# Performance work log

Hardware: AMD Instinct MI355X
Metric: run time of the kernel (lower is better)

## Reference

```python
import jax, jax.numpy as jnp
import numpy as np

D_MODEL = 1024
NUM_HEADS = 16
D_K = D_MODEL // NUM_HEADS
D_FF = 4096
B, S = 4, 2048
EPS = 1e-5


def _linear_params(key, d_in, d_out):
    # torch nn.Linear default init: U(-1/sqrt(d_in), 1/sqrt(d_in))
    k1, k2 = jax.random.split(key)
    bound = 1.0 / np.sqrt(d_in)
    W = jax.random.uniform(k1, (d_in, d_out), jnp.float32, -bound, bound)
    b = jax.random.uniform(k2, (d_out,), jnp.float32, -bound, bound)
    return W, b


def setup_inputs() -> dict:
    key = jax.random.key(0)
    ks = jax.random.split(key, 8)
    x = jax.random.normal(ks[0], (B, S, D_MODEL), jnp.float32)
    Wq, bq = _linear_params(ks[1], D_MODEL, D_MODEL)
    Wk, bk = _linear_params(ks[2], D_MODEL, D_MODEL)
    Wv, bv = _linear_params(ks[3], D_MODEL, D_MODEL)
    Wo, bo = _linear_params(ks[4], D_MODEL, D_MODEL)
    W1, b1 = _linear_params(ks[5], D_MODEL, D_FF)
    W2, b2 = _linear_params(ks[6], D_FF, D_MODEL)
    ln1_g = jnp.ones((D_MODEL,), jnp.float32)
    ln1_b = jnp.zeros((D_MODEL,), jnp.float32)
    ln2_g = jnp.ones((D_MODEL,), jnp.float32)
    ln2_b = jnp.zeros((D_MODEL,), jnp.float32)
    return dict(x=x, Wq=Wq, bq=bq, Wk=Wk, bk=bk, Wv=Wv, bv=bv, Wo=Wo, bo=bo,
                W1=W1, b1=b1, W2=W2, b2=b2,
                ln1_g=ln1_g, ln1_b=ln1_b, ln2_g=ln2_g, ln2_b=ln2_b)


def _layernorm(x, g, b):
    mu = jnp.mean(x, axis=-1, keepdims=True)
    var = jnp.mean(jnp.square(x - mu), axis=-1, keepdims=True)
    return (x - mu) * jax.lax.rsqrt(var + EPS) * g + b


def _attention(h, Wq, bq, Wk, bk, Wv, bv, Wo, bo):
    b, s, _ = h.shape
    def split_heads(t):  # (b,s,d) -> (b,H,s,dk)
        return t.reshape(b, s, NUM_HEADS, D_K).transpose(0, 2, 1, 3)
    Q = split_heads(h @ Wq + bq)
    K = split_heads(h @ Wk + bk)
    V = split_heads(h @ Wv + bv)
    scores = jnp.einsum('bhqd,bhkd->bhqk', Q, K) / np.sqrt(D_K)
    causal = jnp.tril(jnp.ones((s, s), dtype=bool))  # True = keep
    scores = jnp.where(causal, scores, -jnp.inf)
    attn = jax.nn.softmax(scores, axis=-1)
    out = jnp.einsum('bhqk,bhkd->bhqd', attn, V)
    out = out.transpose(0, 2, 1, 3).reshape(b, s, D_MODEL)
    return out @ Wo + bo


def reference(x, Wq, bq, Wk, bk, Wv, bv, Wo, bo, W1, b1, W2, b2,
              ln1_g, ln1_b, ln2_g, ln2_b):
    # pre-norm residual block
    x = x + _attention(_layernorm(x, ln1_g, ln1_b), Wq, bq, Wk, bk, Wv, bv, Wo, bo)
    h = _layernorm(x, ln2_g, ln2_b)
    x = x + (jax.nn.relu(h @ W1 + b1) @ W2 + b2)
    return x
```

## Files before the change

### kernel.cpp

```cpp
#include <hip/hip_runtime.h>
#include <hip/hip_bf16.h>

typedef __bf16 bf16;
typedef __attribute__((ext_vector_type(8))) __bf16 bf16x8;
typedef __attribute__((ext_vector_type(4))) float f32x4;

#define D_MODEL 1024
#define NHEADS  16
#define DK      64
#define DFF     4096
#define BATCH   4
#define SEQ     2048
#define NTOK    (BATCH*SEQ)

__device__ __forceinline__ void gload16(const bf16* g, bf16* l) {
    __builtin_amdgcn_global_load_lds((const __attribute__((address_space(1))) void*)g,
                                     (__attribute__((address_space(3))) void*)l, 16, 0, 0);
}

__device__ __forceinline__ int pack2(float a, float b) {
    union { bf16 h[2]; int i; } u;
    u.h[0] = (bf16)a; u.h[1] = (bf16)b;
    return u.i;
}

__global__ __launch_bounds__(256) void transpose_cast(
    const float* __restrict__ W, bf16* __restrict__ Wt, int K, int N)
{
    __shared__ float tile[32][33];
    const int tx = threadIdx.x, ty = threadIdx.y;
    const int n0 = blockIdx.x * 32, k0 = blockIdx.y * 32;
#pragma unroll
    for (int i = 0; i < 4; ++i)
        tile[ty + i*8][tx] = W[(size_t)(k0 + ty + i*8) * N + n0 + tx];
    __syncthreads();
#pragma unroll
    for (int i = 0; i < 4; ++i)
        Wt[(size_t)(n0 + ty + i*8) * K + k0 + tx] = (bf16)tile[tx][ty + i*8];
}

__global__ __launch_bounds__(256) void transpose_v(
    const bf16* __restrict__ V, bf16* __restrict__ VT)
{
    __shared__ bf16 t[64][72];
    const int bh = blockIdx.y;
    const int s0 = blockIdx.x * 64;
    const int r  = threadIdx.x >> 2;
    const int c0 = (threadIdx.x & 3) * 16;
    const bf16* Vb = V  + (size_t)bh * SEQ * DK;
    bf16*       Tb = VT + (size_t)bh * DK * SEQ;
#pragma unroll
    for (int i = 0; i < 2; ++i) {
        bf16x8 v = *(const bf16x8*)&Vb[(size_t)(s0 + r) * DK + c0 + i*8];
#pragma unroll
        for (int j = 0; j < 8; ++j) t[c0 + i*8 + j][r] = v[j];
    }
    __syncthreads();
#pragma unroll
    for (int i = 0; i < 2; ++i) {
        bf16x8 o;
#pragma unroll
        for (int j = 0; j < 8; ++j) o[j] = t[r][c0 + i*8 + j];
        *(bf16x8*)&Tb[(size_t)r * SEQ + s0 + c0 + i*8] = o;
    }
}

__global__ __launch_bounds__(256) void ln_kernel(
    const float* __restrict__ x, const float* __restrict__ g,
    const float* __restrict__ beta, bf16* __restrict__ out)
{
    const int row = blockIdx.x, tid = threadIdx.x;
    const f32x4* xr = (const f32x4*)(x + (size_t)row * D_MODEL);
    f32x4 v = xr[tid];
    float s  = v[0] + v[1] + v[2] + v[3];
    float s2 = v[0]*v[0] + v[1]*v[1] + v[2]*v[2] + v[3]*v[3];
#pragma unroll
    for (int off = 32; off > 0; off >>= 1) {
        s  += __shfl_down(s,  off, 64);
        s2 += __shfl_down(s2, off, 64);
    }
    __shared__ float red[8];
    const int wave = tid >> 6, lane = tid & 63;
    if (lane == 0) { red[wave] = s; red[wave + 4] = s2; }
    __syncthreads();
    if (tid == 0) {
        float a = red[0] + red[1] + red[2] + red[3];
        float c = red[4] + red[5] + red[6] + red[7];
        float mu  = a * (1.0f / D_MODEL);
        float var = c * (1.0f / D_MODEL) - mu * mu;
        red[0] = mu;
        red[1] = rsqrtf(var + 1e-5f);
    }
    __syncthreads();
    const float mu = red[0], rs = red[1];
    f32x4 gv = ((const f32x4*)g)[tid];
    f32x4 bv = ((const f32x4*)beta)[tid];
    union { bf16 h[4]; uint2 u; } o;
#pragma unroll
    for (int i = 0; i < 4; ++i) o.h[i] = (bf16)((v[i] - mu) * rs * gv[i] + bv[i]);
    *(uint2*)(out + (size_t)row * D_MODEL + tid * 4) = o.u;
}

template<int EPI>
__global__ __launch_bounds__(256, 2) void gemm_bf16(
    const bf16* __restrict__ A, const bf16* __restrict__ Bt,
    const float* __restrict__ bias, const float* __restrict__ resid,
    void* __restrict__ outp, int M, int N, int K)
{
    __shared__ __align__(16) bf16 As[128 * 32];
    __shared__ __align__(16) bf16 Bs[128 * 32];
    const int tid  = threadIdx.x;
    const int wave = tid >> 6, lane = tid & 63;
    const int quad = lane >> 4, l16 = lane & 15;
    const int wr = wave >> 1, wc = wave & 1;
    const int m0 = blockIdx.y * 128, n0 = blockIdx.x * 128;

    const int r0 = wave * 32 + (lane >> 2);
    const int r1 = r0 + 16;
    const int u0 = ((lane & 3) - ((r0 >> 1) & 3)) & 3;
    const int u1 = ((lane & 3) - ((r1 >> 1) & 3)) & 3;
    const bf16* gA0 = A  + (size_t)(m0 + r0) * K + u0 * 8;
    const bf16* gA1 = A  + (size_t)(m0 + r1) * K + u1 * 8;
    const bf16* gB0 = Bt + (size_t)(n0 + r0) * K + u0 * 8;
    const bf16* gB1 = Bt + (size_t)(n0 + r1) * K + u1 * 8;
    bf16* lA0 = As + wave * 1024;
    bf16* lA1 = As + wave * 1024 + 512;
    bf16* lB0 = Bs + wave * 1024;
    bf16* lB1 = Bs + wave * 1024 + 512;

    int aoff[4], boff[4];
#pragma unroll
    for (int i = 0; i < 4; ++i) {
        const int ra = wr * 64 + i * 16 + l16;
        aoff[i] = ra * 32 + ((quad + ((ra >> 1) & 3)) & 3) * 8;
        const int rb = wc * 64 + i * 16 + l16;
        boff[i] = rb * 32 + ((quad + ((rb >> 1) & 3)) & 3) * 8;
    }

    const f32x4 vzero = {0.f, 0.f, 0.f, 0.f};
    f32x4 acc[4][4];
#pragma unroll
    for (int i = 0; i < 4; ++i)
#pragma unroll
        for (int j = 0; j < 4; ++j) acc[i][j] = vzero;

    for (int k0 = 0; k0 < K; k0 += 32) {
        __syncthreads();
        gload16(gA0 + k0, lA0);
        gload16(gA1 + k0, lA1);
        gload16(gB0 + k0, lB0);
        gload16(gB1 + k0, lB1);
        __syncthreads();
        bf16x8 af[4], bfr[4];
#pragma unroll
        for (int i = 0; i < 4; ++i) af[i]  = *(const bf16x8*)&As[aoff[i]];
#pragma unroll
        for (int j = 0; j < 4; ++j) bfr[j] = *(const bf16x8*)&Bs[boff[j]];
#pragma unroll
        for (int i = 0; i < 4; ++i)
#pragma unroll
            for (int j = 0; j < 4; ++j)
                acc[i][j] = __builtin_amdgcn_mfma_f32_16x16x32_bf16(af[i], bfr[j], acc[i][j], 0, 0, 0);
    }

#pragma unroll
    for (int i = 0; i < 4; ++i) {
#pragma unroll
        for (int j = 0; j < 4; ++j) {
            const int col = n0 + wc * 64 + j * 16 + l16;
            const float bcol = bias[col];
#pragma unroll
            for (int r = 0; r < 4; ++r) {
                const int row = m0 + wr * 64 + i * 16 + quad * 4 + r;
                const float v = acc[i][j][r] + bcol;
                if (EPI == 0) {
                    const int bb = row >> 11, ss = row & (SEQ - 1);
                    const int hh = col >> 6,  dd = col & (DK - 1);
                    ((bf16*)outp)[((size_t)(bb * NHEADS + hh) * SEQ + ss) * DK + dd] = (bf16)v;
                } else if (EPI == 1) {
                    const size_t idx = (size_t)row * N + col;
                    ((float*)outp)[idx] = v + resid[idx];
                } else {
                    ((bf16*)outp)[(size_t)row * N + col] = (bf16)fmaxf(v, 0.f);
                }
            }
        }
    }
}

__global__ __launch_bounds__(256, 2) void attn_kernel(
    const bf16* __restrict__ Q, const bf16* __restrict__ K,
    const bf16* __restrict__ VT, bf16* __restrict__ out)
{
    const int bh = blockIdx.y;
    const int b = bh >> 4, h = bh & 15;
    const int tid  = threadIdx.x;
    const int wave = tid >> 6, lane = tid & 63;
    const int quad = lane >> 4, l16 = lane & 15;

    __shared__ __align__(16) bf16 Ks[128 * 72];
    __shared__ __align__(16) bf16 Vt[64 * 136];

    const bf16* Qb = Q  + (size_t)bh * SEQ * DK;
    const bf16* Kb = K  + (size_t)bh * SEQ * DK;
    const bf16* Vb = VT + (size_t)bh * DK * SEQ;

    const int srcA = (2 * (quad & 1)) * 16 + l16;
    const int srcB = srcA + 16;
    const bool thi = quad >= 2;

    const f32x4 vzero = {0.f, 0.f, 0.f, 0.f};

    for (int half = 0; half < 2; ++half) {
        const int qt = half ? (int)blockIdx.x : 15 - (int)blockIdx.x;
        const int qw = qt * 128 + wave * 32;

        bf16x8 qf[2][2];
#pragma unroll
        for (int qi = 0; qi < 2; ++qi)
#pragma unroll
            for (int kk = 0; kk < 2; ++kk)
                qf[qi][kk] = *(const bf16x8*)&Qb[(size_t)(qw + qi*16 + l16) * DK + kk*32 + quad*8];

        f32x4 Oacc[2][4];
        float m_[2], l_[2];
#pragma unroll
        for (int qi = 0; qi < 2; ++qi) {
            m_[qi] = -3.0e38f; l_[qi] = 0.f;
#pragma unroll
            for (int dj = 0; dj < 4; ++dj) Oacc[qi][dj] = vzero;
        }

        const int ntiles = qt + 1;
        for (int t = 0; t < ntiles; ++t) {
            const int kv0 = t * 128;
            __syncthreads();
            for (int c = tid; c < 1024; c += 256) {
                const int r = c >> 3, u = c & 7;
                *(f32x4*)&Ks[r * 72 + u * 8] = *(const f32x4*)&Kb[(size_t)(kv0 + r) * DK + u * 8];
            }
            for (int c = tid; c < 1024; c += 256) {
                const int r = c >> 4, u = c & 15;
                *(f32x4*)&Vt[r * 136 + u * 8] = *(const f32x4*)&Vb[(size_t)r * SEQ + kv0 + u * 8];
            }
            __syncthreads();

            f32x4 sv[8][2];
#pragma unroll
            for (int kvt = 0; kvt < 8; ++kvt) {
                bf16x8 kf0 = *(const bf16x8*)&Ks[(kvt*16 + l16) * 72 + quad*8];
                bf16x8 kf1 = *(const bf16x8*)&Ks[(kvt*16 + l16) * 72 + 32 + quad*8];
#pragma unroll
                for (int qi = 0; qi < 2; ++qi) {
                    f32x4 tacc = vzero;
                    tacc = __builtin_amdgcn_mfma_f32_16x16x32_bf16(kf0, qf[qi][0], tacc, 0, 0, 0);
                    tacc = __builtin_amdgcn_mfma_f32_16x16x32_bf16(kf1, qf[qi][1], tacc, 0, 0, 0);
                    sv[kvt][qi] = tacc;
                }
            }

            const float scale = 0.125f;
            if (t == qt) {
#pragma unroll
                for (int kvt = 0; kvt < 8; ++kvt)
#pragma unroll
                    for (int qi = 0; qi < 2; ++qi)
#pragma unroll
                        for (int r = 0; r < 4; ++r) {
                            const int kv = kv0 + kvt*16 + quad*4 + r;
                            const int q  = qw + qi*16 + l16;
                            sv[kvt][qi][r] = (kv <= q) ? sv[kvt][qi][r] * scale : -3.0e38f;
                        }
            } else {
#pragma unroll
                for (int kvt = 0; kvt < 8; ++kvt)
#pragma unroll
                    for (int qi = 0; qi < 2; ++qi)
#pragma unroll
                        for (int r = 0; r < 4; ++r) sv[kvt][qi][r] *= scale;
            }

#pragma unroll
            for (int qi = 0; qi < 2; ++qi) {
                float mx = sv[0][qi][0];
#pragma unroll
                for (int kvt = 0; kvt < 8; ++kvt)
#pragma unroll
                    for (int r = 0; r < 4; ++r) mx = fmaxf(mx, sv[kvt][qi][r]);
                mx = fmaxf(mx, __shfl_xor(mx, 16, 64));
                mx = fmaxf(mx, __shfl_xor(mx, 32, 64));
                const float newm  = fmaxf(m_[qi], mx);
                const float alpha = __expf(m_[qi] - newm);
                m_[qi] = newm;
                float rs = 0.f;
#pragma unroll
                for (int kvt = 0; kvt < 8; ++kvt)
#pragma unroll
                    for (int r = 0; r < 4; ++r) {
                        const float p = __expf(sv[kvt][qi][r] - newm);
                        sv[kvt][qi][r] = p;
                        rs += p;
                    }
                rs += __shfl_xor(rs, 16, 64);
                rs += __shfl_xor(rs, 32, 64);
                l_[qi] = l_[qi] * alpha + rs;
#pragma unroll
                for (int dj = 0; dj < 4; ++dj) Oacc[qi][dj] *= alpha;
            }

#pragma unroll
            for (int c2 = 0; c2 < 4; ++c2) {
                bf16x8 vf[4];
#pragma unroll
                for (int dj = 0; dj < 4; ++dj)
                    vf[dj] = *(const bf16x8*)&Vt[(dj*16 + l16) * 136 + c2*32 + quad*8];
#pragma unroll
                for (int qi = 0; qi < 2; ++qi) {
                    const int p00 = pack2(sv[2*c2][qi][0],   sv[2*c2][qi][1]);
                    const int p01 = pack2(sv[2*c2][qi][2],   sv[2*c2][qi][3]);
                    const int p10 = pack2(sv[2*c2+1][qi][0], sv[2*c2+1][qi][1]);
                    const int p11 = pack2(sv[2*c2+1][qi][2], sv[2*c2+1][qi][3]);
                    const int a0 = __shfl(p00, srcA, 64), a1 = __shfl(p01, srcA, 64);
                    const int a2 = __shfl(p10, srcA, 64), a3 = __shfl(p11, srcA, 64);
                    const int b0 = __shfl(p00, srcB, 64), b1 = __shfl(p01, srcB, 64);
                    const int b2 = __shfl(p10, srcB, 64), b3 = __shfl(p11, srcB, 64);
                    union { int i[4]; bf16x8 v; } pf;
                    pf.i[0] = thi ? a2 : a0;
                    pf.i[1] = thi ? a3 : a1;
                    pf.i[2] = thi ? b2 : b0;
                    pf.i[3] = thi ? b3 : b1;
#pragma unroll
                    for (int dj = 0; dj < 4; ++dj)
                        Oacc[qi][dj] = __builtin_amdgcn_mfma_f32_16x16x32_bf16(vf[dj], pf.v, Oacc[qi][dj], 0, 0, 0);
                }
            }
        }

#pragma unroll
        for (int qi = 0; qi < 2; ++qi) {
            const float inv = 1.0f / l_[qi];
            const int q = qw + qi*16 + l16;
#pragma unroll
            for (int dj = 0; dj < 4; ++dj)
#pragma unroll
                for (int r = 0; r < 4; ++r) {
                    const int d = dj*16 + quad*4 + r;
                    out[((size_t)(b * SEQ + q)) * D_MODEL + h * DK + d] = (bf16)(Oacc[qi][dj][r] * inv);
                }
        }
    }
}

extern "C" void kernel_launch(void* const* d_in, const int* in_sizes, int n_in,
                              void* d_out, int out_size, void* d_ws, size_t ws_size,
                              hipStream_t stream)
{
    const float* x    = (const float*)d_in[0];
    const float* Wq   = (const float*)d_in[1];
    const float* bq   = (const float*)d_in[2];
    const float* Wk   = (const float*)d_in[3];
    const float* bk   = (const float*)d_in[4];
    const float* Wv   = (const float*)d_in[5];
    const float* bv   = (const float*)d_in[6];
    const float* Wo   = (const float*)d_in[7];
    const float* bo   = (const float*)d_in[8];
    const float* W1   = (const float*)d_in[9];
    const float* b1   = (const float*)d_in[10];
    const float* W2   = (const float*)d_in[11];
    const float* b2   = (const float*)d_in[12];
    const float* ln1g = (const float*)d_in[13];
    const float* ln1b = (const float*)d_in[14];
    const float* ln2g = (const float*)d_in[15];
    const float* ln2b = (const float*)d_in[16];

    char* ws = (char*)d_ws;
    const size_t MB = 1024 * 1024;
    bf16* WTq  = (bf16*)(ws + 0 * MB);
    bf16* WTk  = (bf16*)(ws + 2 * MB);
    bf16* WTv  = (bf16*)(ws + 4 * MB);
    bf16* WTo  = (bf16*)(ws + 6 * MB);
    bf16* WT1  = (bf16*)(ws + 8 * MB);
    bf16* WT2  = (bf16*)(ws + 16 * MB);
    bf16* hbuf = (bf16*)(ws + 24 * MB);
    bf16* VhT  = (bf16*)(ws + 24 * MB);
    bf16* Qh   = (bf16*)(ws + 40 * MB);
    bf16* Kh   = (bf16*)(ws + 56 * MB);
    bf16* Vh   = (bf16*)(ws + 72 * MB);
    bf16* attn = (bf16*)(ws + 88 * MB);
    bf16* ff1  = (bf16*)(ws + 40 * MB);
    float* x2  = (float*)d_out;

    dim3 tb(32, 8);
    transpose_cast<<<dim3(32, 32),  tb, 0, stream>>>(Wq, WTq, 1024, 1024);
    transpose_cast<<<dim3(32, 32),  tb, 0, stream>>>(Wk, WTk, 1024, 1024);
    transpose_cast<<<dim3(32, 32),  tb, 0, stream>>>(Wv, WTv, 1024, 1024);
    transpose_cast<<<dim3(32, 32),  tb, 0, stream>>>(Wo, WTo, 1024, 1024);
    transpose_cast<<<dim3(128, 32), tb, 0, stream>>>(W1, WT1, 1024, 4096);
    transpose_cast<<<dim3(32, 128), tb, 0, stream>>>(W2, WT2, 4096, 1024);

    ln_kernel<<<NTOK, 256, 0, stream>>>(x, ln1g, ln1b, hbuf);

    gemm_bf16<0><<<dim3(8, 64), 256, 0, stream>>>(hbuf, WTq, bq, nullptr, Qh, NTOK, 1024, 1024);
    gemm_bf16<0><<<dim3(8, 64), 256, 0, stream>>>(hbuf, WTk, bk, nullptr, Kh, NTOK, 1024, 1024);
    gemm_bf16<0><<<dim3(8, 64), 256, 0, stream>>>(hbuf, WTv, bv, nullptr, Vh, NTOK, 1024, 1024);

    transpose_v<<<dim3(32, 64), 256, 0, stream>>>(Vh, VhT);

    attn_kernel<<<dim3(8, 64), 256, 0, stream>>>(Qh, Kh, VhT, attn);

    gemm_bf16<1><<<dim3(8, 64), 256, 0, stream>>>(attn, WTo, bo, x, x2, NTOK, 1024, 1024);

    ln_kernel<<<NTOK, 256, 0, stream>>>(x2, ln2g, ln2b, hbuf);

    gemm_bf16<2><<<dim3(32, 64), 256, 0, stream>>>(hbuf, WT1, b1, nullptr, ff1, NTOK, 4096, 1024);
    gemm_bf16<1><<<dim3(8, 64),  256, 0, stream>>>(ff1, WT2, b2, x2, x2, NTOK, 1024, 4096);
}
```

Measured before the change: 571.9 us.

## Fuse QKV projections, fold softmax scale into Q, and restructure attention loads

The three Q/K/V projection GEMMs become one N=3072 launch whose epilogue picks the bias per segment. It writes Q pre-scaled by log2(e)/sqrt(dk) so the attention softmax can use exp2 with no per-score multiply. The attention kernel drops block-wide LDS staging of K and V and its barriers, reading fragments straight from global memory and relying on cache. The P operand now goes through a per-wave LDS buffer instead of cross-lane shuffles. The QKV fusion assumes the WTq, WTk, WTv buffers are contiguous, and the uncached global fragment loads may cost more bandwidth than the removed syncs save.

```diff
diff --git a/kernel.cpp b/kernel.cpp
--- a/kernel.cpp
+++ b/kernel.cpp
@@ -12,16 +12,11 @@
 #define BATCH   4
 #define SEQ     2048
 #define NTOK    (BATCH*SEQ)
+#define QSCALE  0.18033688011112042f
 
 __device__ __forceinline__ void gload16(const bf16* g, bf16* l) {
     __builtin_amdgcn_global_load_lds((const __attribute__((address_space(1))) void*)g,
                                      (__attribute__((address_space(3))) void*)l, 16, 0, 0);
-}
-
-__device__ __forceinline__ int pack2(float a, float b) {
-    union { bf16 h[2]; int i; } u;
-    u.h[0] = (bf16)a; u.h[1] = (bf16)b;
-    return u.i;
 }
 
 __global__ __launch_bounds__(256) void transpose_cast(
@@ -104,7 +99,8 @@
 template<int EPI>
 __global__ __launch_bounds__(256, 2) void gemm_bf16(
     const bf16* __restrict__ A, const bf16* __restrict__ Bt,
-    const float* __restrict__ bias, const float* __restrict__ resid,
+    const float* __restrict__ bias, const float* __restrict__ bias2,
+    const float* __restrict__ bias3, const float* __restrict__ resid,
     void* __restrict__ outp, int M, int N, int K)
 {
     __shared__ __align__(16) bf16 As[128 * 32];
@@ -168,15 +164,24 @@
 #pragma unroll
         for (int j = 0; j < 4; ++j) {
             const int col = n0 + wc * 64 + j * 16 + l16;
-            const float bcol = bias[col];
+            float bcol, sc = 1.0f;
+            if (EPI == 0) {
+                const int seg = col >> 10;
+                const float* bp = (seg == 0) ? bias : ((seg == 1) ? bias2 : bias3);
+                bcol = bp[col & 1023];
+                if (seg == 0) sc = QSCALE;
+            } else {
+                bcol = bias[col];
+            }
 #pragma unroll
             for (int r = 0; r < 4; ++r) {
                 const int row = m0 + wr * 64 + i * 16 + quad * 4 + r;
                 const float v = acc[i][j][r] + bcol;
                 if (EPI == 0) {
                     const int bb = row >> 11, ss = row & (SEQ - 1);
-                    const int hh = col >> 6,  dd = col & (DK - 1);
-                    ((bf16*)outp)[((size_t)(bb * NHEADS + hh) * SEQ + ss) * DK + dd] = (bf16)v;
+                    const int hh = (col & 1023) >> 6, dd = col & (DK - 1);
+                    const size_t seg = (size_t)(col >> 10);
+                    ((bf16*)outp)[seg * 8388608 + (((size_t)(bb * NHEADS + hh)) * SEQ + ss) * DK + dd] = (bf16)(v * sc);
                 } else if (EPI == 1) {
                     const size_t idx = (size_t)row * N + col;
                     ((float*)outp)[idx] = v + resid[idx];
@@ -198,17 +203,13 @@
     const int wave = tid >> 6, lane = tid & 63;
     const int quad = lane >> 4, l16 = lane & 15;
 
-    __shared__ __align__(16) bf16 Ks[128 * 72];
-    __shared__ __align__(16) bf16 Vt[64 * 136];
+    __shared__ __align__(16) bf16 Ps[4][32 * 136];
+    bf16* Pw = Ps[wave];
 
     const bf16* Qb = Q  + (size_t)bh * SEQ * DK;
     const bf16* Kb = K  + (size_t)bh * SEQ * DK;
     const bf16* Vb = VT + (size_t)bh * DK * SEQ;
 
-    const int srcA = (2 * (quad & 1)) * 16 + l16;
-    const int srcB = srcA + 16;
-    const bool thi = quad >= 2;
-
     const f32x4 vzero = {0.f, 0.f, 0.f, 0.f};
 
     for (int half = 0; half < 2; ++half) {
@@ -226,30 +227,20 @@
         float m_[2], l_[2];
 #pragma unroll
         for (int qi = 0; qi < 2; ++qi) {
-            m_[qi] = -3.0e38f; l_[qi] = 0.f;
+            m_[qi] = -1.0e30f; l_[qi] = 0.f;
 #pragma unroll
             for (int dj = 0; dj < 4; ++dj) Oacc[qi][dj] = vzero;
         }
 
-        const int ntiles = qt + 1;
-        for (int t = 0; t < ntiles; ++t) {
+        for (int t = 0; t <= qt; ++t) {
             const int kv0 = t * 128;
-            __syncthreads();
-            for (int c = tid; c < 1024; c += 256) {
-                const int r = c >> 3, u = c & 7;
-                *(f32x4*)&Ks[r * 72 + u * 8] = *(const f32x4*)&Kb[(size_t)(kv0 + r) * DK + u * 8];
-            }
-            for (int c = tid; c < 1024; c += 256) {
-                const int r = c >> 4, u = c & 15;
-                *(f32x4*)&Vt[r * 136 + u * 8] = *(const f32x4*)&Vb[(size_t)r * SEQ + kv0 + u * 8];
-            }
-            __syncthreads();
 
             f32x4 sv[8][2];
 #pragma unroll
             for (int kvt = 0; kvt < 8; ++kvt) {
-                bf16x8 kf0 = *(const bf16x8*)&Ks[(kvt*16 + l16) * 72 + quad*8];
-                bf16x8 kf1 = *(const bf16x8*)&Ks[(kvt*16 + l16) * 72 + 32 + quad*8];
+                const bf16* krow = &Kb[(size_t)(kv0 + kvt*16 + l16) * DK + quad*8];
+                bf16x8 kf0 = *(const bf16x8*)krow;
+                bf16x8 kf1 = *(const bf16x8*)(krow + 32);
 #pragma unroll
                 for (int qi = 0; qi < 2; ++qi) {
                     f32x4 tacc = vzero;
@@ -259,7 +250,6 @@
                 }
             }
 
-            const float scale = 0.125f;
             if (t == qt) {
 #pragma unroll
                 for (int kvt = 0; kvt < 8; ++kvt)
@@ -269,15 +259,8 @@
                         for (int r = 0; r < 4; ++r) {
                             const int kv = kv0 + kvt*16 + quad*4 + r;
                             const int q  = qw + qi*16 + l16;
-                            sv[kvt][qi][r] = (kv <= q) ? sv[kvt][qi][r] * scale : -3.0e38f;
+                            if (kv > q) sv[kvt][qi][r] = -1.0e30f;
                         }
-            } else {
-#pragma unroll
-                for (int kvt = 0; kvt < 8; ++kvt)
-#pragma unroll
-                    for (int qi = 0; qi < 2; ++qi)
-#pragma unroll
-                        for (int r = 0; r < 4; ++r) sv[kvt][qi][r] *= scale;
             }
 
 #pragma unroll
@@ -290,14 +273,14 @@
                 mx = fmaxf(mx, __shfl_xor(mx, 16, 64));
                 mx = fmaxf(mx, __shfl_xor(mx, 32, 64));
                 const float newm  = fmaxf(m_[qi], mx);
-                const float alpha = __expf(m_[qi] - newm);
+                const float alpha = exp2f(m_[qi] - newm);
                 m_[qi] = newm;
                 float rs = 0.f;
 #pragma unroll
                 for (int kvt = 0; kvt < 8; ++kvt)
 #pragma unroll
                     for (int r = 0; r < 4; ++r) {
-                        const float p = __expf(sv[kvt][qi][r] - newm);
+                        const float p = exp2f(sv[kvt][qi][r] - newm);
                         sv[kvt][qi][r] = p;
                         rs += p;
                     }
@@ -309,29 +292,27 @@
             }
 
 #pragma unroll
+            for (int qi = 0; qi < 2; ++qi)
+#pragma unroll
+                for (int kvt = 0; kvt < 8; ++kvt) {
+                    union { bf16 h[4]; unsigned long long u; } pk;
+#pragma unroll
+                    for (int r = 0; r < 4; ++r) pk.h[r] = (bf16)sv[kvt][qi][r];
+                    *(unsigned long long*)&Pw[(qi*16 + l16) * 136 + kvt*16 + quad*4] = pk.u;
+                }
+
+#pragma unroll
             for (int c2 = 0; c2 < 4; ++c2) {
                 bf16x8 vf[4];
 #pragma unroll
                 for (int dj = 0; dj < 4; ++dj)
-                    vf[dj] = *(const bf16x8*)&Vt[(dj*16 + l16) * 136 + c2*32 + quad*8];
+                    vf[dj] = *(const bf16x8*)&Vb[(size_t)(dj*16 + l16) * SEQ + kv0 + c2*32 + quad*8];
 #pragma unroll
                 for (int qi = 0; qi < 2; ++qi) {
-                    const int p00 = pack2(sv[2*c2][qi][0],   sv[2*c2][qi][1]);
-                    const int p01 = pack2(sv[2*c2][qi][2],   sv[2*c2][qi][3]);
-                    const int p10 = pack2(sv[2*c2+1][qi][0], sv[2*c2+1][qi][1]);
-                    const int p11 = pack2(sv[2*c2+1][qi][2], sv[2*c2+1][qi][3]);
-                    const int a0 = __shfl(p00, srcA, 64), a1 = __shfl(p01, srcA, 64);
-                    const int a2 = __shfl(p10, srcA, 64), a3 = __shfl(p11, srcA, 64);
-                    const int b0 = __shfl(p00, srcB, 64), b1 = __shfl(p01, srcB, 64);
-                    const int b2 = __shfl(p10, srcB, 64), b3 = __shfl(p11, srcB, 64);
-                    union { int i[4]; bf16x8 v; } pf;
-                    pf.i[0] = thi ? a2 : a0;
-                    pf.i[1] = thi ? a3 : a1;
-                    pf.i[2] = thi ? b2 : b0;
-                    pf.i[3] = thi ? b3 : b1;
+                    bf16x8 pf = *(const bf16x8*)&Pw[(qi*16 + l16) * 136 + c2*32 + quad*8];
 #pragma unroll
                     for (int dj = 0; dj < 4; ++dj)
-                        Oacc[qi][dj] = __builtin_amdgcn_mfma_f32_16x16x32_bf16(vf[dj], pf.v, Oacc[qi][dj], 0, 0, 0);
+                        Oacc[qi][dj] = __builtin_amdgcn_mfma_f32_16x16x32_bf16(vf[dj], pf, Oacc[qi][dj], 0, 0, 0);
                 }
             }
         }
@@ -400,18 +381,16 @@
 
     ln_kernel<<<NTOK, 256, 0, stream>>>(x, ln1g, ln1b, hbuf);
 
-    gemm_bf16<0><<<dim3(8, 64), 256, 0, stream>>>(hbuf, WTq, bq, nullptr, Qh, NTOK, 1024, 1024);
-    gemm_bf16<0><<<dim3(8, 64), 256, 0, stream>>>(hbuf, WTk, bk, nullptr, Kh, NTOK, 1024, 1024);
-    gemm_bf16<0><<<dim3(8, 64), 256, 0, stream>>>(hbuf, WTv, bv, nullptr, Vh, NTOK, 1024, 1024);
+    gemm_bf16<0><<<dim3(24, 64), 256, 0, stream>>>(hbuf, WTq, bq, bk, bv, nullptr, Qh, NTOK, 3072, 1024);
 
     transpose_v<<<dim3(32, 64), 256, 0, stream>>>(Vh, VhT);
 
     attn_kernel<<<dim3(8, 64), 256, 0, stream>>>(Qh, Kh, VhT, attn);
 
-    gemm_bf16<1><<<dim3(8, 64), 256, 0, stream>>>(attn, WTo, bo, x, x2, NTOK, 1024, 1024);
+    gemm_bf16<1><<<dim3(8, 64), 256, 0, stream>>>(attn, WTo, bo, nullptr, nullptr, x, x2, NTOK, 1024, 1024);
 
     ln_kernel<<<NTOK, 256, 0, stream>>>(x2, ln2g, ln2b, hbuf);
 
-    gemm_bf16<2><<<dim3(32, 64), 256, 0, stream>>>(hbuf, WT1, b1, nullptr, ff1, NTOK, 4096, 1024);
-    gemm_bf16<1><<<dim3(8, 64),  256, 0, stream>>>(ff1, WT2, b2, x2, x2, NTOK, 1024, 4096);
-}
+    gemm_bf16<2><<<dim3(32, 64), 256, 0, stream>>>(hbuf, WT1, b1, nullptr, nullptr, nullptr, ff1, NTOK, 4096, 1024);
+    gemm_bf16<1><<<dim3(8, 64),  256, 0, stream>>>(ff1, WT2, b2, nullptr, nullptr, x2, x2, NTOK, 1024, 4096);
+}
```

After: 597.0 us. 4.4% more time.
